# Performance work log

Hardware: AMD Instinct MI355X
Metric: run time of the kernel (lower is better)

Reference implementation:

```python
import jax, jax.numpy as jnp
import numpy as np
from jax import lax

IN_DIM = 128
B, H, W = 4, 64, 64


def setup_inputs() -> dict:
    key = jax.random.key(0)
    ks = jax.random.split(key, 11)
    C = IN_DIM
    c8 = C // 8
    s = lambda k, shape, scale: jax.random.normal(k, shape, dtype=jnp.float32) * scale
    return {
        "x": s(ks[0], (B, C, H, W), 1.0),
        "x_forward": s(ks[1], (B, C, H, W), 1.0),
        "x_backward": s(ks[2], (B, C, H, W), 1.0),
        # 1x1 conv weights stored as [out, in]
        "Wq": s(ks[3], (c8, C), C ** -0.5),
        "bq": jnp.zeros((c8,), jnp.float32),
        "Wk": s(ks[4], (c8, C), C ** -0.5),
        "bk": jnp.zeros((c8,), jnp.float32),
        "Wv": s(ks[5], (C, C), C ** -0.5),
        "bv": jnp.zeros((C,), jnp.float32),
        # 3x3 conv weight [out=C, in=2C, kh, kw]
        "Wf": s(ks[6], (C, 2 * C, 3, 3), (2 * C * 9) ** -0.5),
        "bf": jnp.zeros((C,), jnp.float32),
    }


def _conv1x1(x, w, b):
    # x: [B,C,H,W], w: [O,C] -> [B,O,H,W]
    return jnp.einsum("bchw,oc->bohw", x, w) + b[None, :, None, None]


def reference(x, x_forward, x_backward, Wq, bq, Wk, bk, Wv, bv, Wf, bf):
    Bb, C, Hh, Ww = x.shape
    HW = Hh * Ww
    query = _conv1x1(x_forward, Wq, bq).reshape(Bb, -1, HW)   # [B,c8,HW]
    key = _conv1x1(x, Wk, bk).reshape(Bb, -1, HW)             # [B,c8,HW]
    value = _conv1x1(x_backward, Wv, bv).reshape(Bb, C, HW)   # [B,C,HW]

    # att_score[b, k_pos, q_pos] = key[b,:,k_pos] . query[b,:,q_pos]
    att_score = jnp.einsum("bck,bcq->bkq", key, query)        # [B,HW,HW]
    max_value = jnp.max(att_score, axis=-1)                   # [B,HW]
    idx = jnp.argmax(att_score, axis=-1)                      # [B,HW] int

    selected_value = jnp.take_along_axis(value, idx[:, None, :], axis=2)
    selected_value = selected_value.reshape(Bb, C, Hh, Ww)
    max_value = max_value.reshape(Bb, 1, Hh, Ww)

    front_res = jnp.concatenate([x, selected_value], axis=1)  # [B,2C,H,W]
    front_res = lax.conv_general_dilated(
        front_res, Wf, window_strides=(1, 1), padding="SAME",
        dimension_numbers=("NCHW", "OIHW", "NCHW"),
    ) + bf[None, :, None, None]
    front_res = front_res * max_value
    return x + front_res
```

## Files before the change

### kernel.cpp

```cpp
#include <hip/hip_runtime.h>

#define HW 4096
#define CC 128
#define MARGIN 2e-3f

typedef unsigned short ushort_t;
typedef unsigned int uint_t;
typedef __attribute__((ext_vector_type(8))) short short8;
typedef __attribute__((ext_vector_type(4))) float f32x4;

__device__ __forceinline__ float dot4(float4 a, float4 b) {
    return (a.x*b.x + a.y*b.y) + (a.z*b.z + a.w*b.w);
}

__device__ __forceinline__ ushort_t f2bf(float f) {
    union { float f; uint_t u; } cv; cv.f = f;
    uint_t r = cv.u + 0x7fffu + ((cv.u >> 16) & 1u);
    return (ushort_t)(r >> 16);
}

__device__ __forceinline__ float bf2f(ushort_t h) {
    union { uint_t u; float f; } cv; cv.u = ((uint_t)h) << 16;
    return cv.f;
}

__device__ __forceinline__ void store16(ushort_t* dst, const ushort_t* s) {
    union { ushort_t s[8]; uint4 v; } a, b;
    #pragma unroll
    for (int j = 0; j < 8; j++) { a.s[j] = s[j]; b.s[j] = s[8+j]; }
    *(uint4*)dst = a.v;
    *(uint4*)(dst + 8) = b.v;
}

__device__ __forceinline__ void gl2lds16(const ushort_t* g, ushort_t* l) {
    __builtin_amdgcn_global_load_lds(
        (const __attribute__((address_space(1))) unsigned int*)g,
        (__attribute__((address_space(3))) unsigned int*)l, 16, 0, 0);
}

__global__ __launch_bounds__(256) void prep_kernel(
    const float* __restrict__ x, const float* __restrict__ xf, const float* __restrict__ xb,
    const float* __restrict__ Wq, const float* __restrict__ bq,
    const float* __restrict__ Wk, const float* __restrict__ bk,
    const float* __restrict__ Wv, const float* __restrict__ bv,
    const float* __restrict__ Wf,
    float* __restrict__ Qt, float* __restrict__ Kt, float* __restrict__ V,
    ushort_t* __restrict__ Qs, ushort_t* __restrict__ KB,
    ushort_t* __restrict__ xsel, ushort_t* __restrict__ Wt)
{
    __shared__ __align__(16) unsigned char smem[16704];
    int bid = blockIdx.x;
    int tid = threadIdx.x;

    if (bid < 256) {
        bool isQ = bid < 128;
        int sub = bid & 127;
        int b = sub >> 5, pt = sub & 31;
        const float* src  = isQ ? xf : x;
        const float* W    = isQ ? Wq : Wk;
        const float* bias = isQ ? bq : bk;
        int ph = tid >> 7, pl = tid & 127;
        int p = pt*128 + pl;
        int pg = (b << 12) + p;
        const float* sp = src + ((size_t)b << 19) + p + ((size_t)(ph*64) << 12);

        float acc[16];
        #pragma unroll
        for (int o = 0; o < 16; o++) acc[o] = ph ? 0.f : bias[o];

        for (int cc = 0; cc < 64; cc += 4) {
            float x0 = sp[(size_t)(cc+0) << 12];
            float x1 = sp[(size_t)(cc+1) << 12];
            float x2 = sp[(size_t)(cc+2) << 12];
            float x3 = sp[(size_t)(cc+3) << 12];
            #pragma unroll
            for (int o = 0; o < 16; o++) {
                float4 w = *(const float4*)&W[o*128 + ph*64 + cc];
                acc[o] += w.x*x0 + w.y*x1 + w.z*x2 + w.w*x3;
            }
        }

        float* sAcc = (float*)smem;
        if (ph) {
            #pragma unroll
            for (int o = 0; o < 16; o++) sAcc[pl*17 + o] = acc[o];
        }
        __syncthreads();
        if (!ph) {
            #pragma unroll
            for (int o = 0; o < 16; o++) acc[o] += sAcc[pl*17 + o];

            float* dstF = isQ ? Qt : Kt;
            float4* df = (float4*)(dstF + (size_t)pg * 16);
            df[0] = make_float4(acc[0],acc[1],acc[2],acc[3]);
            df[1] = make_float4(acc[4],acc[5],acc[6],acc[7]);
            df[2] = make_float4(acc[8],acc[9],acc[10],acc[11]);
            df[3] = make_float4(acc[12],acc[13],acc[14],acc[15]);

            ushort_t h[16], m[16], l[16];
            #pragma unroll
            for (int d = 0; d < 16; d++) {
                h[d] = f2bf(acc[d]);
                float r1 = acc[d] - bf2f(h[d]);
                m[d] = f2bf(r1);
                l[d] = f2bf(r1 - bf2f(m[d]));
            }
            if (isQ) {
                ushort_t* o_ = Qs + (size_t)pg*64;
                store16(o_,      h);
                store16(o_ + 16, m);
                store16(o_ + 32, h);
                store16(o_ + 48, l);
            } else {
                int u = b*256 + (p >> 4);
                int n = p & 15;
                ushort_t* o_ = KB + (size_t)u*1536 + n*32;
                store16(o_,        h); store16(o_ + 16,   h);
                store16(o_ + 512,  m); store16(o_ + 528,  m);
                store16(o_ + 1024, l); store16(o_ + 1040, h);
            }
        }
    } else if (bid < 1280) {
        int vbid = bid - 256;
        int b = vbid >> 8, og = (vbid >> 4) & 15, pt = vbid & 15;
        float* sW = (float*)smem;
        for (int e = tid; e < 1024; e += 256) sW[e] = Wv[og*1024 + e];
        __syncthreads();

        int p = pt*256 + tid;
        const float* sp = xb + ((size_t)b << 19) + p;

        float acc[8];
        #pragma unroll
        for (int j = 0; j < 8; j++) acc[j] = 0.f;

        for (int c4 = 0; c4 < 128; c4 += 4) {
            float x0 = sp[(size_t)(c4+0) << 12];
            float x1 = sp[(size_t)(c4+1) << 12];
            float x2 = sp[(size_t)(c4+2) << 12];
            float x3 = sp[(size_t)(c4+3) << 12];
            #pragma unroll
            for (int j = 0; j < 8; j++) {
                float4 w = *(const float4*)&sW[j*128 + c4];
                acc[j] += w.x*x0 + w.y*x1 + w.z*x2 + w.w*x3;
            }
        }
        float* vr = V + ((size_t)((b << 12) + p))*128 + og*8;
        float4 r0 = make_float4(acc[0]+bv[og*8+0], acc[1]+bv[og*8+1],
                                acc[2]+bv[og*8+2], acc[3]+bv[og*8+3]);
        float4 r1 = make_float4(acc[4]+bv[og*8+4], acc[5]+bv[og*8+5],
                                acc[6]+bv[og*8+6], acc[7]+bv[og*8+7]);
        *(float4*)vr = r0;
        *(float4*)(vr + 4) = r1;
    } else if (bid < 1536) {
        ushort_t* sT = (ushort_t*)smem;
        int xbid = bid - 1280;
        int b = xbid >> 6, y = xbid & 63;
        int cq = tid >> 6, xx = tid & 63;
        const float* src = x + ((size_t)b << 19) + (y << 6) + xx;
        #pragma unroll 4
        for (int k = 0; k < 32; k++) {
            int c = cq*32 + k;
            sT[xx*130 + c] = f2bf(src[(size_t)c << 12]);
        }
        __syncthreads();
        uint_t* dst = (uint_t*)(xsel + ((size_t)(b*4356 + (y+1)*66 + 1))*256);
        #pragma unroll
        for (int k = 0; k < 16; k++) {
            int idx = k*256 + tid;
            int s = idx >> 6, u = idx & 63;
            uint_t v = *(const uint_t*)&sT[s*130 + u*2];
            dst[s*128 + u] = v;
        }
    } else if (bid < 1666) {
        int g = (bid - 1536) * 256 + tid;
        if (g < 33280) {
            int b = g / 8320;
            int rem = g - b * 8320;
            int si = rem >> 5;
            int ch = rem & 31;
            int y, xx;
            if (si < 66)      { y = 0;  xx = si; }
            else if (si < 132){ y = 65; xx = si - 66; }
            else { int t = si - 132; y = 1 + (t >> 1); xx = (t & 1) ? 65 : 0; }
            int site = y * 66 + xx;
            uint4* dst = (uint4*)(xsel + ((size_t)(b*4356 + site))*256);
            dst[ch] = make_uint4(0,0,0,0);
        }
    } else {
        int t = (bid - 1666) * 256 + tid;
        if (t < 36864) {
            int cg = t & 3;
            int o = (t >> 2) & 31;
            int tc = t >> 7;
            int tap = tc % 9;
            int rest = tc / 9;
            int cb = rest & 7, og = rest >> 3;
            union { ushort_t s[8]; uint4 v; } pk;
            #pragma unroll
            for (int j = 0; j < 8; j++) {
                int ci = cg*8 + j;
                pk.s[j] = f2bf(Wf[(size_t)(og*32 + o)*2304 + (cb*32 + ci)*9 + tap]);
            }
            *(uint4*)(Wt + (size_t)t*8) = pk.v;
        }
    }
}

__global__ __launch_bounds__(512, 2) void att_kernel(
    const ushort_t* __restrict__ Qs, const ushort_t* __restrict__ KB,
    float* __restrict__ maxv, int* __restrict__ idxv,
    int* __restrict__ gN, int* __restrict__ gList)
{
    __shared__ float sM1[64*33];
    __shared__ int   sI1[64*33];
    __shared__ float sM2[64*33];

    int bid = blockIdx.x;
    int kg = bid & 63, b = bid >> 6;
    int tid = threadIdx.x;
    int wave = tid >> 6, lane = tid & 63;
    int l15 = lane & 15, quad = lane >> 4;

    short8 Bf[4][3];
    const ushort_t* kb = KB + ((size_t)((b*256 + kg*4)*3))*512 + l15*32 + quad*8;
    #pragma unroll
    for (int t = 0; t < 4; t++)
        #pragma unroll
        for (int p = 0; p < 3; p++)
            Bf[t][p] = *(const short8*)(kb + (size_t)(t*3 + p)*512);

    const ushort_t* qbase = Qs + ((size_t)(b*4096 + wave*512 + l15))*64 + quad*8;

    float m1[4], m2[4]; int i1[4];
    #pragma unroll
    for (int t = 0; t < 4; t++) { m1[t] = -1e30f; m2[t] = -1e30f; i1[t] = 0; }

    for (int it = 0; it < 32; it++) {
        const ushort_t* aptr = qbase + it*1024;
        short8 A1 = *(const short8*)aptr;
        short8 A2 = *(const short8*)(aptr + 32);
        f32x4 acc[4];
        #pragma unroll
        for (int t = 0; t < 4; t++) {
            acc[t] = (f32x4)0.f;
            acc[t] = __builtin_amdgcn_mfma_f32_16x16x32_bf16(A1, Bf[t][0], acc[t], 0, 0, 0);
            acc[t] = __builtin_amdgcn_mfma_f32_16x16x32_bf16(A1, Bf[t][1], acc[t], 0, 0, 0);
            acc[t] = __builtin_amdgcn_mfma_f32_16x16x32_bf16(A2, Bf[t][2], acc[t], 0, 0, 0);
        }
        int q0 = wave*512 + it*16 + quad*4;
        #pragma unroll
        for (int r = 0; r < 4; r++) {
            int cand = q0 + r;
            #pragma unroll
            for (int t = 0; t < 4; t++) {
                float d = acc[t][r];
                float old1 = m1[t];
                bool gt = d > old1;
                m1[t] = gt ? d : old1;
                i1[t] = gt ? cand : i1[t];
                m2[t] = __builtin_amdgcn_fmed3f(d, old1, m2[t]);
            }
        }
    }

    #pragma unroll
    for (int t = 0; t < 4; t++) {
        int kl_ = t*16 + l15;
        int slot = wave*4 + quad;
        sM1[kl_*33 + slot] = m1[t];
        sI1[kl_*33 + slot] = i1[t];
        sM2[kl_*33 + slot] = m2[t];
    }
    __syncthreads();
    if (tid < 64) {
        float M1 = -1e30f; int I1 = 0x7fffffff;
        for (int s = 0; s < 32; s++) {
            float m = sM1[tid*33 + s]; int i = sI1[tid*33 + s];
            if (m > M1 || (m == M1 && i < I1)) { M1 = m; I1 = i; }
        }
        float M2 = -1e30f;
        for (int s = 0; s < 32; s++) {
            float m = sM1[tid*33 + s]; int i = sI1[tid*33 + s];
            float cnd = (i == I1) ? sM2[tid*33 + s] : m;
            M2 = fmaxf(M2, cnd);
        }
        int row = (b << 12) + kg*64 + tid;
        maxv[row] = M1; idxv[row] = I1;
        if (M1 - M2 < MARGIN) {
            int p = atomicAdd(gN, 1);
            gList[p] = row;
        }
    }
}

__global__ __launch_bounds__(256) void fixup2_kernel(
    const float* __restrict__ Qt, const float* __restrict__ Kt,
    const int* __restrict__ gN, const int* __restrict__ gList,
    float* __restrict__ maxv, int* __restrict__ idxv)
{
    __shared__ float sRm[256];
    __shared__ int   sRi[256];
    int n = *gN;
    int tid = threadIdx.x;
    for (int e = blockIdx.x; e < n; e += 64) {
        int r2 = gList[e];
        int b2 = r2 >> 12, k2 = r2 & 4095;
        const float4* Kp = (const float4*)(Kt + ((size_t)(b2*4096 + k2))*16);
        float4 ka = Kp[0], kbv = Kp[1], kc = Kp[2], kd = Kp[3];
        const float4* Qp = (const float4*)(Qt + ((size_t)b2*4096)*16);
        float m = -1e30f; int i = 0;
        #pragma unroll 4
        for (int j = 0; j < 16; j++) {
            int q = tid*16 + j;
            float4 qa = Qp[q*4+0], qb = Qp[q*4+1], qc = Qp[q*4+2], qd = Qp[q*4+3];
            float d = (dot4(ka,qa) + dot4(kbv,qb)) + (dot4(kc,qc) + dot4(kd,qd));
            if (d > m) { m = d; i = q; }
        }
        sRm[tid] = m; sRi[tid] = i;
        __syncthreads();
        #pragma unroll
        for (int s = 128; s > 0; s >>= 1) {
            if (tid < s) {
                float mo = sRm[tid+s]; int io = sRi[tid+s];
                if (mo > sRm[tid] || (mo == sRm[tid] && io < sRi[tid])) {
                    sRm[tid] = mo; sRi[tid] = io;
                }
            }
            __syncthreads();
        }
        if (tid == 0) { maxv[r2] = sRm[0]; idxv[r2] = sRi[0]; }
        __syncthreads();
    }
}

__global__ __launch_bounds__(256) void gather_kernel(
    const float* __restrict__ V, const int* __restrict__ idxv,
    ushort_t* __restrict__ xsel)
{
    int bid = blockIdx.x;
    int b = bid >> 6, pt = bid & 63;
    int tid = threadIdx.x;
    int pp = tid >> 2, cq = tid & 3;
    int p = pt*64 + pp;
    int ip = idxv[(b << 12) + p];
    const float* vrow = V + ((size_t)((b << 12) + ip))*128 + cq*32;
    int site = ((p >> 6) + 1)*66 + (p & 63) + 1;
    ushort_t* dst = xsel + ((size_t)(b*4356 + site))*256 + 128 + cq*32;
    #pragma unroll
    for (int k = 0; k < 4; k++) {
        float4 a = *(const float4*)(vrow + k*8);
        float4 c = *(const float4*)(vrow + k*8 + 4);
        union { ushort_t s[8]; uint4 v; } pk;
        pk.s[0] = f2bf(a.x); pk.s[1] = f2bf(a.y); pk.s[2] = f2bf(a.z); pk.s[3] = f2bf(a.w);
        pk.s[4] = f2bf(c.x); pk.s[5] = f2bf(c.y); pk.s[6] = f2bf(c.z); pk.s[7] = f2bf(c.w);
        *(uint4*)(dst + k*8) = pk.v;
    }
}

__global__ __launch_bounds__(256) void conv_kernel(
    const float* __restrict__ x, const ushort_t* __restrict__ xsel,
    const ushort_t* __restrict__ Wt, const float* __restrict__ bf,
    const float* __restrict__ maxv, float* __restrict__ out)
{
    __shared__ __align__(16) ushort_t sIn[336*32];
    __shared__ __align__(16) ushort_t sW[9*32*32];

    int bid = blockIdx.x;
    int og = bid & 3, tx = (bid >> 2) & 3, ty = (bid >> 4) & 3, b = bid >> 6;
    int tid = threadIdx.x;
    int wave = tid >> 6, lane = tid & 63;
    int l15 = lane & 15, quad = lane >> 4;

    const ushort_t* xsel_base = xsel + ((size_t)(b*4356 + (ty*16)*66 + tx*16))*256;
    const ushort_t* wt_base   = Wt + (size_t)og*8*9216;

    f32x4 acc[4][2];
    #pragma unroll
    for (int mi = 0; mi < 4; mi++)
        #pragma unroll
        for (int ni = 0; ni < 2; ni++) acc[mi][ni] = (f32x4)0.f;

    int l4q = lane >> 2, l4 = lane & 3;

    for (int cb = 0; cb < 8; cb++) {
        if (cb) __syncthreads();
        for (int r = wave; r < 21; r += 4) {
            int site = r*16 + l4q;
            int iy = site / 18, ix = site - iy*18;
            const ushort_t* g = xsel_base + (size_t)(iy*66 + ix)*256 + cb*32 + l4*8;
            gl2lds16(g, &sIn[r*512]);
        }
        for (int r = wave; r < 18; r += 4) {
            const ushort_t* g = wt_base + (size_t)cb*9216 + r*512 + lane*8;
            gl2lds16(g, &sW[r*512]);
        }
        __syncthreads();

        #pragma unroll
        for (int tap = 0; tap < 9; tap++) {
            const int dy = tap / 3, dx = tap % 3;
            short8 B0 = *(const short8*)&sW[(tap*32 +      l15)*32 + quad*8];
            short8 B1 = *(const short8*)&sW[(tap*32 + 16 + l15)*32 + quad*8];
            #pragma unroll
            for (int mi = 0; mi < 4; mi++) {
                int row = wave*4 + mi + dy;
                short8 A = *(const short8*)&sIn[(row*18 + l15 + dx)*32 + quad*8];
                acc[mi][0] = __builtin_amdgcn_mfma_f32_16x16x32_bf16(A, B0, acc[mi][0], 0, 0, 0);
                acc[mi][1] = __builtin_amdgcn_mfma_f32_16x16x32_bf16(A, B1, acc[mi][1], 0, 0, 0);
            }
        }
    }

    int y0 = ty*16, x0 = tx*16;
    const float* xb_ = x   + ((size_t)b << 19);
    float*       ob  = out + ((size_t)b << 19);
    const float* mxb = maxv + (b << 12);
    #pragma unroll
    for (int mi = 0; mi < 4; mi++) {
        int y = y0 + wave*4 + mi;
        int p = (y << 6) + x0 + quad*4;
        float4 mv = *(const float4*)&mxb[p];
        #pragma unroll
        for (int ni = 0; ni < 2; ni++) {
            int o = og*32 + ni*16 + l15;
            float bfo = bf[o];
            float4 xv = *(const float4*)&xb_[((size_t)o << 12) + p];
            float4 r;
            r.x = xv.x + mv.x * (acc[mi][ni][0] + bfo);
            r.y = xv.y + mv.y * (acc[mi][ni][1] + bfo);
            r.z = xv.z + mv.z * (acc[mi][ni][2] + bfo);
            r.w = xv.w + mv.w * (acc[mi][ni][3] + bfo);
            *(float4*)&ob[((size_t)o << 12) + p] = r;
        }
    }
}

extern "C" void kernel_launch(void* const* d_in, const int* in_sizes, int n_in,
                              void* d_out, int out_size, void* d_ws, size_t ws_size,
                              hipStream_t stream) {
    (void)in_sizes; (void)n_in; (void)out_size; (void)ws_size;
    const float* x  = (const float*)d_in[0];
    const float* xf = (const float*)d_in[1];
    const float* xb = (const float*)d_in[2];
    const float* Wq = (const float*)d_in[3];
    const float* bq = (const float*)d_in[4];
    const float* Wk = (const float*)d_in[5];
    const float* bk = (const float*)d_in[6];
    const float* Wv = (const float*)d_in[7];
    const float* bv = (const float*)d_in[8];
    const float* Wf = (const float*)d_in[9];
    const float* bf = (const float*)d_in[10];
    float* out = (float*)d_out;

    float* ws   = (float*)d_ws;
    float* Qt   = ws;
    float* Kt   = Qt + 262144;
    float* V    = Kt + 262144;
    float* mx   = V  + 2097152;
    int*   idxv = (int*)(mx + 16384);
    int*   gN   = (int*)(idxv + 16384);
    int*   gList= gN + 4;
    ushort_t* Qs   = (ushort_t*)(gList + 16384);
    ushort_t* KB   = Qs + 1048576;
    ushort_t* xsel = KB + 1572864;
    ushort_t* Wt   = xsel + 4460544;

    hipMemsetAsync(gN, 0, sizeof(int), stream);
    hipLaunchKernelGGL(prep_kernel,   dim3(1810), dim3(256), 0, stream,
                       x, xf, xb, Wq, bq, Wk, bk, Wv, bv, Wf,
                       Qt, Kt, V, Qs, KB, xsel, Wt);
    hipLaunchKernelGGL(att_kernel,    dim3(256), dim3(512), 0, stream, Qs, KB, mx, idxv, gN, gList);
    hipLaunchKernelGGL(fixup2_kernel, dim3(64),  dim3(256), 0, stream, Qt, Kt, gN, gList, mx, idxv);
    hipLaunchKernelGGL(gather_kernel, dim3(256), dim3(256), 0, stream, V, idxv, xsel);
    hipLaunchKernelGGL(conv_kernel,   dim3(256), dim3(256), 0, stream, x, xsel, Wt, bf, mx, out);
}
```

Before: 173.6 us.

## Fuse fixup into gather, split QK projection wider, double-buffer conv loads

Three changes land together. The near-tie fixup is folded into the gather kernel through per-row flags and per-block local lists, which removes the memset, the global atomic list and a separate kernel launch. The Q/K projection now uses 512 blocks with a four-way channel split and a shared-memory reduction, giving more parallelism. The conv kernel double-buffers its input and weight LDS tiles so the next channel block's async loads overlap the current MFMA work, at the cost of doubling LDS use, which may lower occupancy. Fixup work is now spread over 256 gather blocks rather than 64, so load balance depends on where the flagged rows fall.

```diff
diff --git a/kernel.cpp b/kernel.cpp
--- a/kernel.cpp
+++ b/kernel.cpp
@@ -52,43 +52,47 @@
     int bid = blockIdx.x;
     int tid = threadIdx.x;
 
-    if (bid < 256) {
-        bool isQ = bid < 128;
-        int sub = bid & 127;
-        int b = sub >> 5, pt = sub & 31;
+    if (bid < 512) {
+        bool isQ = bid < 256;
+        int sub = bid & 255;
+        int b = sub >> 6, pt = sub & 63;
         const float* src  = isQ ? xf : x;
         const float* W    = isQ ? Wq : Wk;
         const float* bias = isQ ? bq : bk;
-        int ph = tid >> 7, pl = tid & 127;
-        int p = pt*128 + pl;
+        int ph = tid >> 6, pl = tid & 63;
+        int p = pt*64 + pl;
         int pg = (b << 12) + p;
-        const float* sp = src + ((size_t)b << 19) + p + ((size_t)(ph*64) << 12);
+        const float* sp = src + ((size_t)b << 19) + p + ((size_t)(ph*32) << 12);
 
         float acc[16];
         #pragma unroll
         for (int o = 0; o < 16; o++) acc[o] = ph ? 0.f : bias[o];
 
-        for (int cc = 0; cc < 64; cc += 4) {
+        for (int cc = 0; cc < 32; cc += 4) {
             float x0 = sp[(size_t)(cc+0) << 12];
             float x1 = sp[(size_t)(cc+1) << 12];
             float x2 = sp[(size_t)(cc+2) << 12];
             float x3 = sp[(size_t)(cc+3) << 12];
             #pragma unroll
             for (int o = 0; o < 16; o++) {
-                float4 w = *(const float4*)&W[o*128 + ph*64 + cc];
+                float4 w = *(const float4*)&W[o*128 + ph*32 + cc];
                 acc[o] += w.x*x0 + w.y*x1 + w.z*x2 + w.w*x3;
             }
         }
 
         float* sAcc = (float*)smem;
         if (ph) {
-            #pragma unroll
-            for (int o = 0; o < 16; o++) sAcc[pl*17 + o] = acc[o];
+            float* dst = sAcc + (ph-1)*1088 + pl*17;
+            #pragma unroll
+            for (int o = 0; o < 16; o++) dst[o] = acc[o];
         }
         __syncthreads();
         if (!ph) {
-            #pragma unroll
-            for (int o = 0; o < 16; o++) acc[o] += sAcc[pl*17 + o];
+            const float* s0 = sAcc + pl*17;
+            const float* s1 = sAcc + 1088 + pl*17;
+            const float* s2 = sAcc + 2176 + pl*17;
+            #pragma unroll
+            for (int o = 0; o < 16; o++) acc[o] += s0[o] + s1[o] + s2[o];
 
             float* dstF = isQ ? Qt : Kt;
             float4* df = (float4*)(dstF + (size_t)pg * 16);
@@ -120,8 +124,8 @@
                 store16(o_ + 1024, l); store16(o_ + 1040, h);
             }
         }
-    } else if (bid < 1280) {
-        int vbid = bid - 256;
+    } else if (bid < 1536) {
+        int vbid = bid - 512;
         int b = vbid >> 8, og = (vbid >> 4) & 15, pt = vbid & 15;
         float* sW = (float*)smem;
         for (int e = tid; e < 1024; e += 256) sW[e] = Wv[og*1024 + e];
@@ -152,9 +156,9 @@
                                 acc[6]+bv[og*8+6], acc[7]+bv[og*8+7]);
         *(float4*)vr = r0;
         *(float4*)(vr + 4) = r1;
-    } else if (bid < 1536) {
+    } else if (bid < 1792) {
         ushort_t* sT = (ushort_t*)smem;
-        int xbid = bid - 1280;
+        int xbid = bid - 1536;
         int b = xbid >> 6, y = xbid & 63;
         int cq = tid >> 6, xx = tid & 63;
         const float* src = x + ((size_t)b << 19) + (y << 6) + xx;
@@ -172,8 +176,8 @@
             uint_t v = *(const uint_t*)&sT[s*130 + u*2];
             dst[s*128 + u] = v;
         }
-    } else if (bid < 1666) {
-        int g = (bid - 1536) * 256 + tid;
+    } else if (bid < 1922) {
+        int g = (bid - 1792) * 256 + tid;
         if (g < 33280) {
             int b = g / 8320;
             int rem = g - b * 8320;
@@ -188,7 +192,7 @@
             dst[ch] = make_uint4(0,0,0,0);
         }
     } else {
-        int t = (bid - 1666) * 256 + tid;
+        int t = (bid - 1922) * 256 + tid;
         if (t < 36864) {
             int cg = t & 3;
             int o = (t >> 2) & 31;
@@ -209,8 +213,7 @@
 
 __global__ __launch_bounds__(512, 2) void att_kernel(
     const ushort_t* __restrict__ Qs, const ushort_t* __restrict__ KB,
-    float* __restrict__ maxv, int* __restrict__ idxv,
-    int* __restrict__ gN, int* __restrict__ gList)
+    float* __restrict__ maxv, int* __restrict__ idxv, int* __restrict__ flags)
 {
     __shared__ float sM1[64*33];
     __shared__ int   sI1[64*33];
@@ -287,28 +290,44 @@
         }
         int row = (b << 12) + kg*64 + tid;
         maxv[row] = M1; idxv[row] = I1;
-        if (M1 - M2 < MARGIN) {
-            int p = atomicAdd(gN, 1);
-            gList[p] = row;
-        }
-    }
-}
-
-__global__ __launch_bounds__(256) void fixup2_kernel(
-    const float* __restrict__ Qt, const float* __restrict__ Kt,
-    const int* __restrict__ gN, const int* __restrict__ gList,
-    float* __restrict__ maxv, int* __restrict__ idxv)
+        flags[row] = (M1 - M2 < MARGIN) ? 1 : 0;
+    }
+}
+
+__global__ __launch_bounds__(256) void gather_kernel(
+    const float* __restrict__ V, const float* __restrict__ Qt,
+    const float* __restrict__ Kt, const int* __restrict__ idxv,
+    const int* __restrict__ flags, float* __restrict__ maxv,
+    ushort_t* __restrict__ xsel)
 {
+    __shared__ int sIdx[64];
+    __shared__ int sFlag[64];
+    __shared__ int sCnt;
     __shared__ float sRm[256];
     __shared__ int   sRi[256];
-    int n = *gN;
+
+    int bid = blockIdx.x;
+    int b = bid >> 6, pt = bid & 63;
     int tid = threadIdx.x;
-    for (int e = blockIdx.x; e < n; e += 64) {
-        int r2 = gList[e];
-        int b2 = r2 >> 12, k2 = r2 & 4095;
-        const float4* Kp = (const float4*)(Kt + ((size_t)(b2*4096 + k2))*16);
+    if (tid == 0) sCnt = 0;
+    __syncthreads();
+    if (tid < 64) {
+        int row = (b << 12) + pt*64 + tid;
+        sIdx[tid] = idxv[row];
+        if (flags[row]) {
+            int s = atomicAdd(&sCnt, 1);
+            sFlag[s] = tid;
+        }
+    }
+    __syncthreads();
+
+    int n = sCnt;
+    for (int e = 0; e < n; e++) {
+        int local = sFlag[e];
+        int row = (b << 12) + pt*64 + local;
+        const float4* Kp = (const float4*)(Kt + (size_t)row*16);
         float4 ka = Kp[0], kbv = Kp[1], kc = Kp[2], kd = Kp[3];
-        const float4* Qp = (const float4*)(Qt + ((size_t)b2*4096)*16);
+        const float4* Qp = (const float4*)(Qt + ((size_t)b << 12)*16);
         float m = -1e30f; int i = 0;
         #pragma unroll 4
         for (int j = 0; j < 16; j++) {
@@ -329,21 +348,16 @@
             }
             __syncthreads();
         }
-        if (tid == 0) { maxv[r2] = sRm[0]; idxv[r2] = sRi[0]; }
+        if (tid == 0) {
+            maxv[row] = sRm[0];
+            sIdx[local] = sRi[0];
+        }
         __syncthreads();
     }
-}
-
-__global__ __launch_bounds__(256) void gather_kernel(
-    const float* __restrict__ V, const int* __restrict__ idxv,
-    ushort_t* __restrict__ xsel)
-{
-    int bid = blockIdx.x;
-    int b = bid >> 6, pt = bid & 63;
-    int tid = threadIdx.x;
+
     int pp = tid >> 2, cq = tid & 3;
     int p = pt*64 + pp;
-    int ip = idxv[(b << 12) + p];
+    int ip = sIdx[pp];
     const float* vrow = V + ((size_t)((b << 12) + ip))*128 + cq*32;
     int site = ((p >> 6) + 1)*66 + (p & 63) + 1;
     ushort_t* dst = xsel + ((size_t)(b*4356 + site))*256 + 128 + cq*32;
@@ -363,8 +377,8 @@
     const ushort_t* __restrict__ Wt, const float* __restrict__ bf,
     const float* __restrict__ maxv, float* __restrict__ out)
 {
-    __shared__ __align__(16) ushort_t sIn[336*32];
-    __shared__ __align__(16) ushort_t sW[9*32*32];
+    __shared__ __align__(16) ushort_t sIn[2][336*32];
+    __shared__ __align__(16) ushort_t sW[2][9*32*32];
 
     int bid = blockIdx.x;
     int og = bid & 3, tx = (bid >> 2) & 3, ty = (bid >> 4) & 3, b = bid >> 6;
@@ -383,33 +397,48 @@
 
     int l4q = lane >> 2, l4 = lane & 3;
 
+    for (int r = wave; r < 21; r += 4) {
+        int site = r*16 + l4q;
+        int iy = site / 18, ix = site - iy*18;
+        const ushort_t* g = xsel_base + (size_t)(iy*66 + ix)*256 + l4*8;
+        gl2lds16(g, &sIn[0][r*512]);
+    }
+    for (int r = wave; r < 18; r += 4) {
+        const ushort_t* g = wt_base + r*512 + lane*8;
+        gl2lds16(g, &sW[0][r*512]);
+    }
+    __syncthreads();
+
     for (int cb = 0; cb < 8; cb++) {
-        if (cb) __syncthreads();
-        for (int r = wave; r < 21; r += 4) {
-            int site = r*16 + l4q;
-            int iy = site / 18, ix = site - iy*18;
-            const ushort_t* g = xsel_base + (size_t)(iy*66 + ix)*256 + cb*32 + l4*8;
-            gl2lds16(g, &sIn[r*512]);
-        }
-        for (int r = wave; r < 18; r += 4) {
-            const ushort_t* g = wt_base + (size_t)cb*9216 + r*512 + lane*8;
-            gl2lds16(g, &sW[r*512]);
-        }
-        __syncthreads();
+        int cur = cb & 1;
+        if (cb < 7) {
+            int nb = cur ^ 1;
+            for (int r = wave; r < 21; r += 4) {
+                int site = r*16 + l4q;
+                int iy = site / 18, ix = site - iy*18;
+                const ushort_t* g = xsel_base + (size_t)(iy*66 + ix)*256 + (cb+1)*32 + l4*8;
+                gl2lds16(g, &sIn[nb][r*512]);
+            }
+            for (int r = wave; r < 18; r += 4) {
+                const ushort_t* g = wt_base + (size_t)(cb+1)*9216 + r*512 + lane*8;
+                gl2lds16(g, &sW[nb][r*512]);
+            }
+        }
 
         #pragma unroll
         for (int tap = 0; tap < 9; tap++) {
             const int dy = tap / 3, dx = tap % 3;
-            short8 B0 = *(const short8*)&sW[(tap*32 +      l15)*32 + quad*8];
-            short8 B1 = *(const short8*)&sW[(tap*32 + 16 + l15)*32 + quad*8];
+            short8 B0 = *(const short8*)&sW[cur][(tap*32 +      l15)*32 + quad*8];
+            short8 B1 = *(const short8*)&sW[cur][(tap*32 + 16 + l15)*32 + quad*8];
             #pragma unroll
             for (int mi = 0; mi < 4; mi++) {
                 int row = wave*4 + mi + dy;
-                short8 A = *(const short8*)&sIn[(row*18 + l15 + dx)*32 + quad*8];
+                short8 A = *(const short8*)&sIn[cur][(row*18 + l15 + dx)*32 + quad*8];
                 acc[mi][0] = __builtin_amdgcn_mfma_f32_16x16x32_bf16(A, B0, acc[mi][0], 0, 0, 0);
                 acc[mi][1] = __builtin_amdgcn_mfma_f32_16x16x32_bf16(A, B1, acc[mi][1], 0, 0, 0);
             }
         }
+        __syncthreads();
     }
 
     int y0 = ty*16, x0 = tx*16;
@@ -459,19 +488,17 @@
     float* V    = Kt + 262144;
     float* mx   = V  + 2097152;
     int*   idxv = (int*)(mx + 16384);
-    int*   gN   = (int*)(idxv + 16384);
-    int*   gList= gN + 4;
-    ushort_t* Qs   = (ushort_t*)(gList + 16384);
+    int*   flags= (int*)(idxv + 16384);
+    ushort_t* Qs   = (ushort_t*)(flags + 16384);
     ushort_t* KB   = Qs + 1048576;
     ushort_t* xsel = KB + 1572864;
     ushort_t* Wt   = xsel + 4460544;
 
-    hipMemsetAsync(gN, 0, sizeof(int), stream);
-    hipLaunchKernelGGL(prep_kernel,   dim3(1810), dim3(256), 0, stream,
+    hipLaunchKernelGGL(prep_kernel,   dim3(2066), dim3(256), 0, stream,
                        x, xf, xb, Wq, bq, Wk, bk, Wv, bv, Wf,
                        Qt, Kt, V, Qs, KB, xsel, Wt);
-    hipLaunchKernelGGL(att_kernel,    dim3(256), dim3(512), 0, stream, Qs, KB, mx, idxv, gN, gList);
-    hipLaunchKernelGGL(fixup2_kernel, dim3(64),  dim3(256), 0, stream, Qt, Kt, gN, gList, mx, idxv);
-    hipLaunchKernelGGL(gather_kernel, dim3(256), dim3(256), 0, stream, V, idxv, xsel);
+    hipLaunchKernelGGL(att_kernel,    dim3(256), dim3(512), 0, stream, Qs, KB, mx, idxv, flags);
+    hipLaunchKernelGGL(gather_kernel, dim3(256), dim3(256), 0, stream,
+                       V, Qt, Kt, idxv, flags, mx, xsel);
     hipLaunchKernelGGL(conv_kernel,   dim3(256), dim3(256), 0, stream, x, xsel, Wt, bf, mx, out);
 }
```

Result: faster. 170.0 us (-2.1%).
